# Kernel tuning notes

Measured on AMD Instinct MI355X. Metric: run time of the kernel, lower is better.

The kernel has to match this reference:

```python
import jax, jax.numpy as jnp
import numpy as np

B, N_REG, D_IN = 32, 116, 256
N_NODES = B * N_REG            # 3712
E_PER_G = N_REG * 10           # avg degree 10
E = B * E_PER_G                # 37120
HEADS = 8
HID = [256, 128, 64]
D_OUT = 256
LN_EPS = 1e-5


def _layer_norm(x, scale, bias):
    mu = x.mean(-1, keepdims=True)
    var = ((x - mu) ** 2).mean(-1, keepdims=True)
    return (x - mu) * jax.lax.rsqrt(var + LN_EPS) * scale + bias


def _gat_layer(x, W, b, a_src, a_dst, src, dst, concat):
    """PyG-style GATConv (shared lin, self-loops, leaky_relu 0.2) + ELU + LayerNorm."""
    N = x.shape[0]
    H, C = a_src.shape
    h = (x @ W).reshape(N, H, C)                      # (N, H, C)
    sl = jnp.arange(N, dtype=src.dtype)               # self-loops (PyG default)
    s = jnp.concatenate([src, sl])
    d = jnp.concatenate([dst, sl])
    al = (h * a_src).sum(-1)                          # (N, H)
    ar = (h * a_dst).sum(-1)                          # (N, H)
    e = jax.nn.leaky_relu(al[s] + ar[d], 0.2)         # (E', H)
    m = jax.ops.segment_max(e, d, num_segments=N)
    ex = jnp.exp(e - m[d])
    den = jax.ops.segment_sum(ex, d, num_segments=N)
    alpha = ex / den[d]                               # segment softmax over incoming edges
    out = jax.ops.segment_sum(h[s] * alpha[..., None], d, num_segments=N)  # (N, H, C)
    out = out.reshape(N, H * C) if concat else out.mean(1)
    return out + b


def setup_inputs() -> dict:
    key = jax.random.key(0)
    ks = list(jax.random.split(key, 32))
    node_features = jax.random.normal(ks[0], (N_NODES, D_IN), dtype=jnp.float32)
    # edges: random within each graph (disconnected batched graph)
    off = (jnp.arange(B, dtype=jnp.int32) * N_REG)[:, None]
    src = (jax.random.randint(ks[1], (B, E_PER_G), 0, N_REG, dtype=jnp.int32) + off).reshape(-1)
    dst = (jax.random.randint(ks[2], (B, E_PER_G), 0, N_REG, dtype=jnp.int32) + off).reshape(-1)
    batch = jnp.repeat(jnp.arange(B, dtype=jnp.int32), N_REG)

    def lin(k, fin, fout):
        s = 1.0 / np.sqrt(fin)
        return jax.random.uniform(k, (fin, fout), jnp.float32, -s, s)

    dims_in = [D_IN, HID[0] * HEADS, HID[1] * HEADS]
    p = {}
    ki = 3
    for i, (fin, c) in enumerate(zip(dims_in, HID)):
        concat = i < len(HID) - 1
        wdim = c * HEADS
        p[f"w{i}"] = lin(ks[ki], fin, wdim); ki += 1
        p[f"b{i}"] = jnp.zeros((wdim if concat else c,), jnp.float32)
        p[f"as{i}"] = jax.random.normal(ks[ki], (HEADS, c), jnp.float32) * 0.1; ki += 1
        p[f"ad{i}"] = jax.random.normal(ks[ki], (HEADS, c), jnp.float32) * 0.1; ki += 1
        ldim = wdim if concat else c
        p[f"ls{i}"] = jnp.ones((ldim,), jnp.float32)
        p[f"lb{i}"] = jnp.zeros((ldim,), jnp.float32)
    p["wp"] = lin(ks[ki], HID[-1], D_OUT); ki += 1
    p["bp"] = jnp.zeros((D_OUT,), jnp.float32)
    p["lsp"] = jnp.ones((D_OUT,), jnp.float32)
    p["lbp"] = jnp.zeros((D_OUT,), jnp.float32)
    p["wq"] = lin(ks[ki], D_OUT, 1); ki += 1
    p["bq"] = jnp.zeros((1,), jnp.float32)
    return dict(node_features=node_features, src=src, dst=dst, batch=batch, **p)


def reference(node_features, src, dst, batch,
              w0, b0, as0, ad0, ls0, lb0,
              w1, b1, as1, ad1, ls1, lb1,
              w2, b2, as2, ad2, ls2, lb2,
              wp, bp, lsp, lbp, wq, bq):
    x = node_features
    x = _layer_norm(jax.nn.elu(_gat_layer(x, w0, b0, as0, ad0, src, dst, True)), ls0, lb0)
    x = _layer_norm(jax.nn.elu(_gat_layer(x, w1, b1, as1, ad1, src, dst, True)), ls1, lb1)
    x = _layer_norm(jax.nn.elu(_gat_layer(x, w2, b2, as2, ad2, src, dst, False)), ls2, lb2)
    node_out = jax.nn.gelu(_layer_norm(x @ wp + bp, lsp, lbp), approximate=False)  # (N, 256)
    pool_w = jax.nn.softmax(node_out @ wq + bq, axis=0)                            # (N, 1) global softmax
    num = jax.ops.segment_sum(node_out * pool_w, batch, num_segments=B)            # (B, 256)
    den = jnp.maximum(jax.ops.segment_sum(pool_w, batch, num_segments=B), 1e-8)    # (B, 1)
    graph_features = num / den
    return graph_features, node_out
```

## Files before the change

### kernel.cpp

```cpp
#include <hip/hip_runtime.h>
#include <hip/hip_bf16.h>
#include <math.h>

typedef __hip_bfloat16 bf16;
typedef short short8 __attribute__((ext_vector_type(8)));
typedef float f32x4 __attribute__((ext_vector_type(4)));

__device__ __forceinline__ float b2f(const bf16 v) { return __bfloat162float(v); }
__device__ __forceinline__ bf16 f2b(const float v) { return __float2bfloat16(v); }

__device__ __forceinline__ float bits2f(short s) {
  unsigned u = ((unsigned)(unsigned short)s) << 16;
  float f;
  __builtin_memcpy(&f, &u, 4);
  return f;
}
__device__ __forceinline__ short f2bits(float f) {
  bf16 b = f2b(f);
  short s;
  __builtin_memcpy(&s, &b, 2);
  return s;
}

__device__ __forceinline__ float ldsel(const void* p, size_t i, int f32) {
  return f32 ? ((const float*)p)[i] : b2f(((const bf16*)p)[i]);
}
__device__ __forceinline__ void stsel(void* p, size_t i, float v, int f32) {
  if (f32) ((float*)p)[i] = v; else ((bf16*)p)[i] = f2b(v);
}

__device__ __forceinline__ void load8f(const void* p, int idx, int f32, float* o) {
  if (f32) {
    const float4* q = (const float4*)((const float*)p + idx);
    float4 a = q[0], b = q[1];
    o[0] = a.x; o[1] = a.y; o[2] = a.z; o[3] = a.w;
    o[4] = b.x; o[5] = b.y; o[6] = b.z; o[7] = b.w;
  } else {
    union { short8 v; short s[8]; } u;
    u.v = *(const short8*)((const bf16*)p + idx);
#pragma unroll
    for (int j = 0; j < 8; ++j) o[j] = bits2f(u.s[j]);
  }
}

#define NN 3712
#define NE 37120
#define NG 32
#define NREG 116
#define MAXDEG 48


__global__ __launch_bounds__(256) void k_detect(const void* nf, const void* w0, int* flags) {
  __shared__ int bad[2];
  if (threadIdx.x < 2) bad[threadIdx.x] = 0;
  __syncthreads();
  const bf16* a = (const bf16*)nf;
  const bf16* b = (const bf16*)w0;
  int l0 = 0, l1 = 0;
  for (int i = threadIdx.x; i < 4096; i += 256) {
    float x = b2f(a[i]); if (!(fabsf(x) < 1e4f)) l0++;
    float y = b2f(b[i]); if (!(fabsf(y) < 1e4f)) l1++;
  }
  if (l0) atomicAdd(&bad[0], l0);
  if (l1) atomicAdd(&bad[1], l1);
  __syncthreads();
  if (threadIdx.x == 0) { flags[0] = bad[0] > 0; flags[1] = bad[1] > 0; }
}

__global__ __launch_bounds__(256) void k_zero(int* __restrict__ p, int n) {
  int i = blockIdx.x * 256 + threadIdx.x;
  if (i < n) p[i] = 0;
}

__global__ __launch_bounds__(256) void k_scatter(const int* __restrict__ src, const int* __restrict__ dst,
                                                 int* __restrict__ cnt, int* __restrict__ bucket, int E) {
  int e = blockIdx.x * 256 + threadIdx.x;
  if (e < E) {
    int d = dst[e], s = src[e];
    if ((unsigned)d < NN && (unsigned)s < NN) {
      int p = atomicAdd(&cnt[d], 1);
      if (p < MAXDEG) bucket[d * MAXDEG + p] = s;
    }
  }
}

__global__ __launch_bounds__(256) void k_tox0(const void* __restrict__ in, bf16* __restrict__ out,
                                              const int* __restrict__ flags) {
  int f = flags[0];
  int bid = blockIdx.x;
  int n = (bid & 7) * 464 + (bid >> 3);
  int i = n * 256 + threadIdx.x;
  out[i] = f2b(ldsel(in, i, f));
}

__global__ __launch_bounds__(256) void k_transpose(const void* __restrict__ W, bf16* __restrict__ Wt,
                                                   int K, int N, const int* __restrict__ flags) {
  int f = flags[1];
  __shared__ float tile[32][33];
  int tx = threadIdx.x & 31, ty = threadIdx.x >> 5;
  int k0 = blockIdx.x * 32, n0 = blockIdx.y * 32;
#pragma unroll
  for (int i = 0; i < 4; ++i)
    tile[ty + i * 8][tx] = ldsel(W, (size_t)(k0 + ty + i * 8) * N + n0 + tx, f);
  __syncthreads();
#pragma unroll
  for (int i = 0; i < 4; ++i)
    Wt[(size_t)(n0 + ty + i * 8) * K + k0 + tx] = f2b(tile[tx][ty + i * 8]);
}

__global__ __launch_bounds__(256) void k_gemm_mfma(const bf16* __restrict__ A, const bf16* __restrict__ Bt,
                                                   bf16* __restrict__ C, int M, int N, int K) {
  __shared__ short As[64 * 72];
  __shared__ short Bs[64 * 72];
  int tid = threadIdx.x;
  int wave = tid >> 6, lane = tid & 63;
  int wr = wave >> 1, wc = wave & 1;
  int quad = lane >> 4, ml = lane & 15;

  int nbx = N >> 6;
  int total = gridDim.x;
  int id = blockIdx.x;
  int tile = ((total & 7) == 0) ? ((id & 7) * (total >> 3) + (id >> 3)) : id;
  int n0 = (tile % nbx) << 6;
  int m0 = (tile / nbx) << 6;

  f32x4 acc[2][2];
#pragma unroll
  for (int rt = 0; rt < 2; ++rt)
#pragma unroll
    for (int ct = 0; ct < 2; ++ct)
#pragma unroll
      for (int r = 0; r < 4; ++r) acc[rt][ct][r] = 0.f;

  for (int k0 = 0; k0 < K; k0 += 64) {
    __syncthreads();
#pragma unroll
    for (int i = 0; i < 2; ++i) {
      int c = tid + (i << 8);
      int row = c >> 3, kg = (c & 7) << 3;
      *(uint4*)&As[row * 72 + kg] = *(const uint4*)&A[(size_t)(m0 + row) * K + k0 + kg];
      *(uint4*)&Bs[row * 72 + kg] = *(const uint4*)&Bt[(size_t)(n0 + row) * K + k0 + kg];
    }
    __syncthreads();
    short8 af[2][2], bfr[2][2];
#pragma unroll
    for (int rt = 0; rt < 2; ++rt)
#pragma unroll
      for (int kk = 0; kk < 2; ++kk)
        af[rt][kk] = *(const short8*)&As[(wr * 32 + rt * 16 + ml) * 72 + kk * 32 + quad * 8];
#pragma unroll
    for (int ct = 0; ct < 2; ++ct)
#pragma unroll
      for (int kk = 0; kk < 2; ++kk)
        bfr[ct][kk] = *(const short8*)&Bs[(wc * 32 + ct * 16 + ml) * 72 + kk * 32 + quad * 8];
#pragma unroll
    for (int rt = 0; rt < 2; ++rt)
#pragma unroll
      for (int ct = 0; ct < 2; ++ct)
#pragma unroll
        for (int kk = 0; kk < 2; ++kk)
          acc[rt][ct] = __builtin_amdgcn_mfma_f32_16x16x32_bf16(af[rt][kk], bfr[ct][kk], acc[rt][ct], 0, 0, 0);
  }
#pragma unroll
  for (int rt = 0; rt < 2; ++rt)
#pragma unroll
    for (int ct = 0; ct < 2; ++ct)
#pragma unroll
      for (int r = 0; r < 4; ++r) {
        int grow = m0 + wr * 32 + rt * 16 + quad * 4 + r;
        int gcol = n0 + wc * 32 + ct * 16 + ml;
        C[(size_t)grow * N + gcol] = f2b(acc[rt][ct][r]);
      }
}

__global__ void k_attn(const bf16* __restrict__ H, const void* __restrict__ a_s,
                       const void* __restrict__ a_d, float* __restrict__ al,
                       float* __restrict__ ar, int C, const int* __restrict__ flags) {
  int wF = flags[1];
  int t = threadIdx.x;
  int D = 8 * C;
  int i0 = t * 8;
  int bid = blockIdx.x;
  int nb = (bid & 7) * 58 + (bid >> 3);
  float as8[8], ad8[8];
  load8f(a_s, i0, wF, as8);
  load8f(a_d, i0, wF, ad8);
  int G = C >> 3;
  int hd = i0 / C;
  for (int it = 0; it < 8; ++it) {
    int n = nb * 8 + it;
    union { short8 v; short s[8]; } u;
    u.v = *(const short8*)&H[(size_t)n * D + i0];
    float ps = 0.f, pd = 0.f;
#pragma unroll
    for (int j = 0; j < 8; ++j) {
      float h = bits2f(u.s[j]);
      ps = fmaf(h, as8[j], ps);
      pd = fmaf(h, ad8[j], pd);
    }
    for (int off = G >> 1; off; off >>= 1) {
      ps += __shfl_xor(ps, off);
      pd += __shfl_xor(pd, off);
    }
    if ((t & (G - 1)) == 0) {
      al[n * 8 + hd] = ps;
      ar[n * 8 + hd] = pd;
    }
  }
}

__global__ __launch_bounds__(256) void k_edgew(const float* __restrict__ al, const float* __restrict__ ar,
                                               const int* __restrict__ cnt, const int* __restrict__ bucket,
                                               float* __restrict__ mbuf, float* __restrict__ ibuf) {
  int t = threadIdx.x;
  int q = t >> 6, l = t & 63, hd = l >> 3, el = l & 7;
  int bid = blockIdx.x;
  int d = (bid & 7) * 464 + (bid >> 3) * 4 + q;
  int deg = cnt[d]; deg = deg > MAXDEG ? MAXDEG : deg;
  int total = deg + 1;
  float ard = ar[d * 8 + hd];
  float lgv[7];
  float m = -1e30f;
#pragma unroll
  for (int k = 0; k < 7; ++k) {
    int e = el + k * 8;
    float lg = -1e30f;
    if (e < total) {
      int s = e < deg ? bucket[d * MAXDEG + e] : d;
      lg = al[s * 8 + hd] + ard;
      lg = lg > 0.f ? lg : 0.2f * lg;
    }
    lgv[k] = lg;
    m = fmaxf(m, lg);
  }
#pragma unroll
  for (int off = 4; off; off >>= 1) m = fmaxf(m, __shfl_xor(m, off));
  float den = 0.f;
#pragma unroll
  for (int k = 0; k < 7; ++k) den += (lgv[k] > -1e29f) ? expf(lgv[k] - m) : 0.f;
#pragma unroll
  for (int off = 4; off; off >>= 1) den += __shfl_xor(den, off);
  if (el == 0) { mbuf[d * 8 + hd] = m; ibuf[d * 8 + hd] = 1.f / den; }
}

template<int C>
__global__ __launch_bounds__(256, 1) void k_aggm(const bf16* __restrict__ H,
    const float* __restrict__ al, const float* __restrict__ ar,
    const float* __restrict__ mbuf, const float* __restrict__ ibuf,
    const int* __restrict__ cnt, const int* __restrict__ bucket,
    bf16* __restrict__ Y) {
  constexpr int D = 8 * C;
  constexpr int KP = 136;
  __shared__ short P[128 * KP];
  __shared__ short Ht[C * KP];
  int t = threadIdx.x;
  int bid = blockIdx.x;
  int x = bid & 7, j = bid >> 3;
  int g = x * 4 + (j & 3);
  int h = j >> 2;
  int gbase = g * NREG;

  short8 z = {0, 0, 0, 0, 0, 0, 0, 0};
  for (int i = t; i < 128 * KP / 8; i += 256) *(short8*)&P[i * 8] = z;
  for (int i = t; i < C * 12; i += 256) {
    int c = i / 12, s = 116 + i % 12;
    Ht[c * KP + (s ^ (((c >> 3) & 15) << 3))] = 0;
  }
  __syncthreads();

  constexpr int CH = C / 8;
  for (int idx = t; idx < NREG * CH; idx += 256) {
    int s = idx / CH, c0 = (idx % CH) * 8;
    int msk = ((idx % CH) & 15) << 3;
    int sw = s ^ msk;
    union { short8 v; short x2[8]; } u;
    u.v = *(const short8*)&H[(size_t)(gbase + s) * D + h * C + c0];
#pragma unroll
    for (int jj = 0; jj < 8; ++jj) Ht[(c0 + jj) * KP + sw] = u.x2[jj];
  }
  if (t < NREG) {
    int gd = gbase + t;
    int deg = cnt[gd]; deg = deg > MAXDEG ? MAXDEG : deg;
    int total = deg + 1;
    float ard = ar[gd * 8 + h];
    float mm = mbuf[gd * 8 + h], inv = ibuf[gd * 8 + h];
    for (int base = 0; base < total; base += 8) {
      int sg[8]; float av[8];
#pragma unroll
      for (int jj = 0; jj < 8; ++jj) {
        int e = base + jj;
        sg[jj] = (e < deg) ? bucket[gd * MAXDEG + e] : gd;
      }
#pragma unroll
      for (int jj = 0; jj < 8; ++jj) av[jj] = al[sg[jj] * 8 + h];
#pragma unroll
      for (int jj = 0; jj < 8; ++jj) {
        if (base + jj < total) {
          float lg = av[jj] + ard;
          lg = lg > 0.f ? lg : 0.2f * lg;
          float alpha = expf(lg - mm) * inv;
          int off = t * KP + (sg[jj] - gbase);
          P[off] = f2bits(bits2f(P[off]) + alpha);
        }
      }
    }
  }
  __syncthreads();

  constexpr int CT = C / 32;
  int wave = t >> 6, lane = t & 63;
  int wr = wave >> 1, wc = wave & 1;
  int quad = lane >> 4, ml = lane & 15;
  f32x4 acc[4][CT];
#pragma unroll
  for (int a = 0; a < 4; ++a)
#pragma unroll
    for (int b = 0; b < CT; ++b)
#pragma unroll
      for (int r = 0; r < 4; ++r) acc[a][b][r] = 0.f;
#pragma unroll
  for (int ks = 0; ks < 4; ++ks) {
    short8 af[4], bf8[CT];
#pragma unroll
    for (int rt = 0; rt < 4; ++rt)
      af[rt] = *(const short8*)&P[(wr * 64 + rt * 16 + ml) * KP + ks * 32 + quad * 8];
#pragma unroll
    for (int ct = 0; ct < CT; ++ct) {
      int cdim = wc * (C / 2) + ct * 16 + ml;
      int msk = ((cdim >> 3) & 15) << 3;
      bf8[ct] = *(const short8*)&Ht[cdim * KP + ((ks * 32 + quad * 8) ^ msk)];
    }
#pragma unroll
    for (int rt = 0; rt < 4; ++rt)
#pragma unroll
      for (int ct = 0; ct < CT; ++ct)
        acc[rt][ct] = __builtin_amdgcn_mfma_f32_16x16x32_bf16(af[rt], bf8[ct], acc[rt][ct], 0, 0, 0);
  }
#pragma unroll
  for (int rt = 0; rt < 4; ++rt) {
    int m2 = wr * 64 + rt * 16 + quad * 4;
#pragma unroll
    for (int r = 0; r < 4; ++r) {
      if (m2 + r < NREG) {
#pragma unroll
        for (int ct = 0; ct < CT; ++ct) {
          int n = wc * (C / 2) + ct * 16 + ml;
          Y[(size_t)(gbase + m2 + r) * D + h * C + n] = f2b(acc[rt][ct][r]);
        }
      }
    }
  }
}

template<int D>
__global__ __launch_bounds__(256) void k_ln(bf16* __restrict__ X, const void* __restrict__ bias,
                                            const void* __restrict__ ls, const void* __restrict__ lb,
                                            const int* __restrict__ flags) {
  int wF = flags[1];
  constexpr int VPT = D / 256;
  int t = threadIdx.x;
  int bid = blockIdx.x;
  int nb = (bid & 7) * 58 + (bid >> 3);
  int node = nb * 8 + (t >> 5);
  int l32 = t & 31;
  float v[VPT * 8];
  float s1 = 0.f, s2 = 0.f;
#pragma unroll
  for (int j = 0; j < VPT; ++j) {
    int c0 = (l32 + j * 32) * 8;
    union { short8 u; short x[8]; } uu;
    uu.u = *(const short8*)&X[(size_t)node * D + c0];
    float bb[8];
    load8f(bias, c0, wF, bb);
#pragma unroll
    for (int k = 0; k < 8; ++k) {
      float vv = bits2f(uu.x[k]) + bb[k];
      vv = vv > 0.f ? vv : expf(vv) - 1.f;
      v[j * 8 + k] = vv; s1 += vv; s2 += vv * vv;
    }
  }
#pragma unroll
  for (int off = 16; off; off >>= 1) { s1 += __shfl_xor(s1, off); s2 += __shfl_xor(s2, off); }
  float mu = s1 / D;
  float rs = rsqrtf(s2 / D - mu * mu + 1e-5f);
#pragma unroll
  for (int j = 0; j < VPT; ++j) {
    int c0 = (l32 + j * 32) * 8;
    float g8[8], b8[8];
    load8f(ls, c0, wF, g8);
    load8f(lb, c0, wF, b8);
    union { short8 u; short x[8]; } uu;
#pragma unroll
    for (int k = 0; k < 8; ++k)
      uu.x[k] = f2bits((v[j * 8 + k] - mu) * rs * g8[k] + b8[k]);
    *(short8*)&X[(size_t)node * D + c0] = uu.u;
  }
}

__global__ void k_agg(const bf16* __restrict__ H, const float* __restrict__ al,
                      const float* __restrict__ ar, const float* __restrict__ mbuf,
                      const float* __restrict__ ibuf, const int* __restrict__ cnt,
                      const int* __restrict__ bucket, const void* __restrict__ bias,
                      const void* __restrict__ ls, const void* __restrict__ lb,
                      bf16* __restrict__ Xout, int C, int concat,
                      const int* __restrict__ flags) {
  int wF = flags[1];
  int bid = blockIdx.x;
  int d = (bid & 7) * 464 + (bid >> 3);
  int t = threadIdx.x;
  int D = 8 * C;
  __shared__ int sid[MAXDEG + 4];
  __shared__ float vals[512];

  int deg = cnt[d]; deg = deg > MAXDEG ? MAXDEG : deg;
  int total = deg + 1;
  int padded = (total + 3) & ~3;
  if (t < padded) sid[t] = t < deg ? bucket[d * MAXDEG + t] : d;
  __syncthreads();

  int i0 = t * 8;
  int hd = i0 / C;
  float m = mbuf[d * 8 + hd], inv = ibuf[d * 8 + hd], ard = ar[d * 8 + hd];

  float acc[8] = {0.f, 0.f, 0.f, 0.f, 0.f, 0.f, 0.f, 0.f};
  const bf16* __restrict__ Hp = H + i0;
  for (int eb = 0; eb < padded; eb += 4) {
    int s4[4]; float a4[4]; short8 u4[4];
#pragma unroll
    for (int j = 0; j < 4; ++j) s4[j] = sid[eb + j];
#pragma unroll
    for (int j = 0; j < 4; ++j) {
      a4[j] = al[s4[j] * 8 + hd];
      u4[j] = *(const short8*)&Hp[(size_t)s4[j] * D];
    }
#pragma unroll
    for (int j = 0; j < 4; ++j) {
      float lg = a4[j] + ard;
      lg = lg > 0.f ? lg : 0.2f * lg;
      float we = (eb + j) < total ? expf(lg - m) * inv : 0.f;
      union { short8 v; short s[8]; } uu; uu.v = u4[j];
#pragma unroll
      for (int k2 = 0; k2 < 8; ++k2) acc[k2] = fmaf(we, bits2f(uu.s[k2]), acc[k2]);
    }
  }

#pragma unroll
  for (int j = 0; j < 8; ++j) vals[i0 + j] = acc[j];
  __syncthreads();
  float v = 0.f;
#pragma unroll
  for (int h = 0; h < 8; ++h) v += vals[h * 64 + t];
  v = v * 0.125f + ldsel(bias, t, wF);
  v = v > 0.f ? v : expf(v) - 1.f;
  float s1 = v, s2 = v * v;
#pragma unroll
  for (int off = 32; off; off >>= 1) { s1 += __shfl_xor(s1, off); s2 += __shfl_xor(s2, off); }
  float mu = s1 * (1.f / 64.f);
  float var = s2 * (1.f / 64.f) - mu * mu;
  float rs = rsqrtf(var + 1e-5f);
  Xout[(size_t)d * 64 + t] = f2b((v - mu) * rs * ldsel(ls, t, wF) + ldsel(lb, t, wF));
}

__global__ __launch_bounds__(256) void k_proj(const bf16* __restrict__ X3, const void* __restrict__ wp,
                                              const void* __restrict__ bp, const void* __restrict__ lsp,
                                              const void* __restrict__ lbp, const void* __restrict__ wq,
                                              const void* __restrict__ bq,
                                              float* __restrict__ q, void* __restrict__ dout,
                                              const int* __restrict__ flags) {
  int wF = flags[1], xF = flags[0];
  int bid = blockIdx.x;
  int n = (bid & 7) * 464 + (bid >> 3);
  int t = threadIdx.x;
  int lane = t & 63, wave = t >> 6;
  __shared__ float xs[64];
  __shared__ float r1[4], r2[4];
  __shared__ float sMu, sRs;
  if (t < 64) xs[t] = b2f(X3[n * 64 + t]);
  __syncthreads();
  float y = ldsel(bp, t, wF);
#pragma unroll 8
  for (int k = 0; k < 64; ++k) y = fmaf(xs[k], ldsel(wp, k * 256 + t, wF), y);
  float s1 = y, s2 = y * y;
#pragma unroll
  for (int off = 32; off; off >>= 1) { s1 += __shfl_down(s1, off); s2 += __shfl_down(s2, off); }
  if (lane == 0) { r1[wave] = s1; r2[wave] = s2; }
  __syncthreads();
  if (t == 0) {
    float S1 = r1[0] + r1[1] + r1[2] + r1[3];
    float S2 = r2[0] + r2[1] + r2[2] + r2[3];
    float mu = S1 / 256.f;
    sMu = mu; sRs = rsqrtf(S2 / 256.f - mu * mu + 1e-5f);
  }
  __syncthreads();
  float v = (y - sMu) * sRs * ldsel(lsp, t, wF) + ldsel(lbp, t, wF);
  float g = 0.5f * v * (1.f + erff(v * 0.70710678118654752f));
  stsel(dout, (size_t)NG * 256 + (size_t)n * 256 + t, g, xF);
  float qv = g * ldsel(wq, t, wF);
#pragma unroll
  for (int off = 32; off; off >>= 1) qv += __shfl_down(qv, off);
  if (lane == 0) r1[wave] = qv;
  __syncthreads();
  if (t == 0) q[n] = r1[0] + r1[1] + r1[2] + r1[3] + ldsel(bq, 0, wF);
}

__global__ __launch_bounds__(256) void k_pool(void* __restrict__ dout, const float* __restrict__ q,
                                              const int* __restrict__ flags) {
  int xF = flags[0];
  int bid = blockIdx.x;
  int b = (bid & 7) * 4 + (bid >> 3);
  int t = threadIdx.x;
  __shared__ float es[NREG];
  __shared__ float sDen;
  if (t < NREG) es[t] = q[b * NREG + t];
  __syncthreads();
  if (t == 0) {
    float m = -1e30f;
    for (int i = 0; i < NREG; ++i) m = fmaxf(m, es[i]);
    float den = 0.f;
    for (int i = 0; i < NREG; ++i) { float e = expf(es[i] - m); es[i] = e; den += e; }
    sDen = den;
  }
  __syncthreads();
  float acc = 0.f;
  for (int i = 0; i < NREG; ++i)
    acc = fmaf(es[i], ldsel(dout, (size_t)NG * 256 + (size_t)(b * NREG + i) * 256 + t, xF), acc);
  stsel(dout, (size_t)b * 256 + t, acc / sDen, xF);
}

extern "C" void kernel_launch(void* const* d_in, const int* in_sizes, int n_in,
                              void* d_out, int out_size, void* d_ws, size_t ws_size,
                              hipStream_t stream) {
  const void* nf  = d_in[0];
  const int* src  = (const int*)d_in[1];
  const int* dst  = (const int*)d_in[2];
  const void *w0 = d_in[4],  *b0 = d_in[5],  *as0 = d_in[6], *ad0 = d_in[7],  *ls0 = d_in[8],  *lb0 = d_in[9];
  const void *w1 = d_in[10], *b1 = d_in[11], *as1 = d_in[12], *ad1 = d_in[13], *ls1 = d_in[14], *lb1 = d_in[15];
  const void *w2 = d_in[16], *b2 = d_in[17], *as2 = d_in[18], *ad2 = d_in[19], *ls2 = d_in[20], *lb2 = d_in[21];
  const void *wp = d_in[22], *bp = d_in[23], *lsp = d_in[24], *lbp = d_in[25], *wq = d_in[26], *bq = d_in[27];

  int* flags  = (int*)d_ws;
  float* al   = (float*)(flags + 4);
  float* ar   = al + NN * 8;
  int* cnt    = (int*)(ar + NN * 8);
  int* bucket = cnt + NN;
  float* q    = (float*)(bucket + NN * MAXDEG);
  bf16* X     = (bf16*)(q + NN);
  bf16* Hb    = X + (size_t)NN * 2048;

  float* mbuf = (float*)d_out;
  float* ibuf = mbuf + NN * 8;

  bf16* X0  = X;
  bf16* wt0 = X + (1 << 20);
  bf16* wt1 = Hb + (size_t)NN * 1024;
  bf16* wt2 = Hb + (size_t)NN * 512;

  k_detect<<<1, 256, 0, stream>>>(nf, w0, flags);
  k_zero<<<(NN + 255) / 256, 256, 0, stream>>>(cnt, NN);
  k_scatter<<<(NE + 255) / 256, 256, 0, stream>>>(src, dst, cnt, bucket, NE);
  k_tox0<<<NN, 256, 0, stream>>>(nf, X0, flags);

  k_transpose<<<dim3(256 / 32, 2048 / 32), 256, 0, stream>>>(w0, wt0, 256, 2048, flags);
  k_gemm_mfma<<<(2048 / 64) * (NN / 64), 256, 0, stream>>>(X0, wt0, Hb, NN, 2048, 256);
  k_attn<<<NN / 8, 256, 0, stream>>>(Hb, as0, ad0, al, ar, 256, flags);
  k_edgew<<<NN / 4, 256, 0, stream>>>(al, ar, cnt, bucket, mbuf, ibuf);
  k_aggm<256><<<256, 256, 0, stream>>>(Hb, al, ar, mbuf, ibuf, cnt, bucket, X);
  k_ln<2048><<<NN / 8, 256, 0, stream>>>(X, b0, ls0, lb0, flags);

  k_transpose<<<dim3(2048 / 32, 1024 / 32), 256, 0, stream>>>(w1, wt1, 2048, 1024, flags);
  k_gemm_mfma<<<(1024 / 64) * (NN / 64), 256, 0, stream>>>(X, wt1, Hb, NN, 1024, 2048);
  k_attn<<<NN / 8, 128, 0, stream>>>(Hb, as1, ad1, al, ar, 128, flags);
  k_edgew<<<NN / 4, 256, 0, stream>>>(al, ar, cnt, bucket, mbuf, ibuf);
  k_aggm<128><<<256, 256, 0, stream>>>(Hb, al, ar, mbuf, ibuf, cnt, bucket, X);
  k_ln<1024><<<NN / 8, 256, 0, stream>>>(X, b1, ls1, lb1, flags);

  k_transpose<<<dim3(1024 / 32, 512 / 32), 256, 0, stream>>>(w2, wt2, 1024, 512, flags);
  k_gemm_mfma<<<(512 / 64) * (NN / 64), 256, 0, stream>>>(X, wt2, Hb, NN, 512, 1024);
  k_attn<<<NN / 8, 64, 0, stream>>>(Hb, as2, ad2, al, ar, 64, flags);
  k_edgew<<<NN / 4, 256, 0, stream>>>(al, ar, cnt, bucket, mbuf, ibuf);
  k_agg<<<NN, 64, 0, stream>>>(Hb, al, ar, mbuf, ibuf, cnt, bucket, b2, ls2, lb2, X, 64, 0, flags);

  k_proj<<<NN, 256, 0, stream>>>(X, wp, bp, lsp, lbp, wq, bq, q, d_out, flags);
  k_pool<<<NG, 256, 0, stream>>>(d_out, q, flags);
}
```

Baseline: 329.7 us.

## Fuse attention-logit reduction into GEMM epilogue and merge prep kernels

Computes the per-head attention logits (al/ar) inside the GEMM epilogue from the fp32 accumulators, using shuffles and atomicAdd into zeroed buffers. This removes the separate k_attn pass that re-read the projected features. The setup kernels (detect, zero, scatter, convert, transpose) are merged into two launches, and the next layer's weight transpose plus the al/ar zeroing are folded into the LayerNorm launch. The aim is fewer launches and less memory traffic, at the cost of float atomics, non-deterministic summation order, and logits taken from unrounded fp32 accumulators rather than bf16 values.

```diff
diff --git a/kernel.cpp b/kernel.cpp
--- a/kernel.cpp
+++ b/kernel.cpp
@@ -50,55 +50,33 @@
 #define MAXDEG 48
 
 
-__global__ __launch_bounds__(256) void k_detect(const void* nf, const void* w0, int* flags) {
-  __shared__ int bad[2];
-  if (threadIdx.x < 2) bad[threadIdx.x] = 0;
-  __syncthreads();
-  const bf16* a = (const bf16*)nf;
-  const bf16* b = (const bf16*)w0;
-  int l0 = 0, l1 = 0;
-  for (int i = threadIdx.x; i < 4096; i += 256) {
-    float x = b2f(a[i]); if (!(fabsf(x) < 1e4f)) l0++;
-    float y = b2f(b[i]); if (!(fabsf(y) < 1e4f)) l1++;
-  }
-  if (l0) atomicAdd(&bad[0], l0);
-  if (l1) atomicAdd(&bad[1], l1);
-  __syncthreads();
-  if (threadIdx.x == 0) { flags[0] = bad[0] > 0; flags[1] = bad[1] > 0; }
-}
-
-__global__ __launch_bounds__(256) void k_zero(int* __restrict__ p, int n) {
-  int i = blockIdx.x * 256 + threadIdx.x;
-  if (i < n) p[i] = 0;
-}
-
-__global__ __launch_bounds__(256) void k_scatter(const int* __restrict__ src, const int* __restrict__ dst,
-                                                 int* __restrict__ cnt, int* __restrict__ bucket, int E) {
-  int e = blockIdx.x * 256 + threadIdx.x;
-  if (e < E) {
-    int d = dst[e], s = src[e];
-    if ((unsigned)d < NN && (unsigned)s < NN) {
-      int p = atomicAdd(&cnt[d], 1);
-      if (p < MAXDEG) bucket[d * MAXDEG + p] = s;
-    }
-  }
-}
-
-__global__ __launch_bounds__(256) void k_tox0(const void* __restrict__ in, bf16* __restrict__ out,
-                                              const int* __restrict__ flags) {
-  int f = flags[0];
-  int bid = blockIdx.x;
-  int n = (bid & 7) * 464 + (bid >> 3);
-  int i = n * 256 + threadIdx.x;
-  out[i] = f2b(ldsel(in, i, f));
-}
-
-__global__ __launch_bounds__(256) void k_transpose(const void* __restrict__ W, bf16* __restrict__ Wt,
-                                                   int K, int N, const int* __restrict__ flags) {
-  int f = flags[1];
-  __shared__ float tile[32][33];
+__global__ __launch_bounds__(256) void k_prep1(const void* nf, const void* w0,
+                                               int* flags, int* cnt) {
+  if (blockIdx.x == 0) {
+    __shared__ int bad[2];
+    if (threadIdx.x < 2) bad[threadIdx.x] = 0;
+    __syncthreads();
+    const bf16* a = (const bf16*)nf;
+    const bf16* b = (const bf16*)w0;
+    int l0 = 0, l1 = 0;
+    for (int i = threadIdx.x; i < 4096; i += 256) {
+      float x = b2f(a[i]); if (!(fabsf(x) < 1e4f)) l0++;
+      float y = b2f(b[i]); if (!(fabsf(y) < 1e4f)) l1++;
+    }
+    if (l0) atomicAdd(&bad[0], l0);
+    if (l1) atomicAdd(&bad[1], l1);
+    __syncthreads();
+    if (threadIdx.x == 0) { flags[0] = bad[0] > 0; flags[1] = bad[1] > 0; }
+  } else {
+    int i = (blockIdx.x - 1) * 256 + threadIdx.x;
+    if (i < NN) cnt[i] = 0;
+  }
+}
+
+__device__ __forceinline__ void dev_transpose(const void* W, bf16* Wt, int K, int N,
+                                              int bx, int by, int f, float tile[32][33]) {
   int tx = threadIdx.x & 31, ty = threadIdx.x >> 5;
-  int k0 = blockIdx.x * 32, n0 = blockIdx.y * 32;
+  int k0 = bx * 32, n0 = by * 32;
 #pragma unroll
   for (int i = 0; i < 4; ++i)
     tile[ty + i * 8][tx] = ldsel(W, (size_t)(k0 + ty + i * 8) * N + n0 + tx, f);
@@ -108,8 +86,40 @@
     Wt[(size_t)(n0 + ty + i * 8) * K + k0 + tx] = f2b(tile[tx][ty + i * 8]);
 }
 
+__global__ __launch_bounds__(256) void k_prep2(const int* __restrict__ src, const int* __restrict__ dst,
+    int* __restrict__ cnt, int* __restrict__ bucket, const void* __restrict__ nf, bf16* __restrict__ X0,
+    const void* __restrict__ w0, bf16* __restrict__ wt0, float* __restrict__ al, float* __restrict__ ar,
+    const int* __restrict__ flags) {
+  __shared__ float tile[32][33];
+  int id = blockIdx.x, t = threadIdx.x;
+  if (id < 145) {
+    int e = id * 256 + t;
+    if (e < NE) {
+      int d = dst[e], s = src[e];
+      if ((unsigned)d < NN && (unsigned)s < NN) {
+        int p = atomicAdd(&cnt[d], 1);
+        if (p < MAXDEG) bucket[d * MAXDEG + p] = s;
+      }
+    }
+  } else if ((id -= 145) < NN) {
+    int f = flags[0];
+    int n = (id & 7) * 464 + (id >> 3);
+    int i = n * 256 + t;
+    X0[i] = f2b(ldsel(nf, i, f));
+  } else if ((id -= NN) < 512) {
+    dev_transpose(w0, wt0, 256, 2048, id & 7, id >> 3, flags[1], tile);
+  } else {
+    id -= 512;
+    int i = id * 256 + t;
+    if (i < NN * 8) { al[i] = 0.f; ar[i] = 0.f; }
+  }
+}
+
 __global__ __launch_bounds__(256) void k_gemm_mfma(const bf16* __restrict__ A, const bf16* __restrict__ Bt,
-                                                   bf16* __restrict__ C, int M, int N, int K) {
+                                                   bf16* __restrict__ C, int M, int N, int K,
+                                                   const void* __restrict__ a_s, const void* __restrict__ a_d,
+                                                   float* __restrict__ al, float* __restrict__ ar,
+                                                   int Chead, const int* __restrict__ flags) {
   __shared__ short As[64 * 72];
   __shared__ short Bs[64 * 72];
   int tid = threadIdx.x;
@@ -171,41 +181,46 @@
         int gcol = n0 + wc * 32 + ct * 16 + ml;
         C[(size_t)grow * N + gcol] = f2b(acc[rt][ct][r]);
       }
-}
-
-__global__ void k_attn(const bf16* __restrict__ H, const void* __restrict__ a_s,
-                       const void* __restrict__ a_d, float* __restrict__ al,
-                       float* __restrict__ ar, int C, const int* __restrict__ flags) {
+
   int wF = flags[1];
-  int t = threadIdx.x;
-  int D = 8 * C;
-  int i0 = t * 8;
-  int bid = blockIdx.x;
-  int nb = (bid & 7) * 58 + (bid >> 3);
-  float as8[8], ad8[8];
-  load8f(a_s, i0, wF, as8);
-  load8f(a_d, i0, wF, ad8);
-  int G = C >> 3;
-  int hd = i0 / C;
-  for (int it = 0; it < 8; ++it) {
-    int n = nb * 8 + it;
-    union { short8 v; short s[8]; } u;
-    u.v = *(const short8*)&H[(size_t)n * D + i0];
-    float ps = 0.f, pd = 0.f;
-#pragma unroll
-    for (int j = 0; j < 8; ++j) {
-      float h = bits2f(u.s[j]);
-      ps = fmaf(h, as8[j], ps);
-      pd = fmaf(h, ad8[j], pd);
-    }
-    for (int off = G >> 1; off; off >>= 1) {
-      ps += __shfl_xor(ps, off);
-      pd += __shfl_xor(pd, off);
-    }
-    if ((t & (G - 1)) == 0) {
-      al[n * 8 + hd] = ps;
-      ar[n * 8 + hd] = pd;
-    }
+  int hd = n0 / Chead;
+  float asv[2], adv[2];
+#pragma unroll
+  for (int ct = 0; ct < 2; ++ct) {
+    int gcol = n0 + wc * 32 + ct * 16 + ml;
+    asv[ct] = ldsel(a_s, gcol, wF);
+    adv[ct] = ldsel(a_d, gcol, wF);
+  }
+  float pal[8], par[8];
+#pragma unroll
+  for (int k = 0; k < 8; ++k) { pal[k] = 0.f; par[k] = 0.f; }
+#pragma unroll
+  for (int rt = 0; rt < 2; ++rt)
+#pragma unroll
+    for (int ct = 0; ct < 2; ++ct)
+#pragma unroll
+      for (int r = 0; r < 4; ++r) {
+        int k = rt * 4 + r;
+        pal[k] = fmaf(acc[rt][ct][r], asv[ct], pal[k]);
+        par[k] = fmaf(acc[rt][ct][r], adv[ct], par[k]);
+      }
+#pragma unroll
+  for (int off = 1; off < 16; off <<= 1) {
+#pragma unroll
+    for (int k = 0; k < 8; ++k) {
+      pal[k] += __shfl_xor(pal[k], off);
+      par[k] += __shfl_xor(par[k], off);
+    }
+  }
+  if (ml == 0) {
+#pragma unroll
+    for (int rt = 0; rt < 2; ++rt)
+#pragma unroll
+      for (int r = 0; r < 4; ++r) {
+        int grow = m0 + wr * 32 + rt * 16 + quad * 4 + r;
+        atomicAdd(&al[grow * 8 + hd], pal[rt * 4 + r]);
+        atomicAdd(&ar[grow * 8 + hd], par[rt * 4 + r]);
+      }
   }
 }
 
@@ -352,14 +367,24 @@
   }
 }
 
-template<int D>
+template<int D, int TK, int TN>
 __global__ __launch_bounds__(256) void k_ln(bf16* __restrict__ X, const void* __restrict__ bias,
                                             const void* __restrict__ ls, const void* __restrict__ lb,
+                                            float* __restrict__ al, float* __restrict__ ar,
+                                            const void* __restrict__ W, bf16* __restrict__ Wt,
                                             const int* __restrict__ flags) {
+  __shared__ float tile[32][33];
+  int bid = blockIdx.x;
+  if (bid >= 464) {
+    int id = bid - 464;
+    dev_transpose(W, Wt, TK, TN, id % (TK / 32), id / (TK / 32), flags[1], tile);
+    return;
+  }
+  int gid = bid * 256 + threadIdx.x;
+  if (gid < NN * 8) { al[gid] = 0.f; ar[gid] = 0.f; }
   int wF = flags[1];
   constexpr int VPT = D / 256;
   int t = threadIdx.x;
-  int bid = blockIdx.x;
   int nb = (bid & 7) * 58 + (bid >> 3);
   int node = nb * 8 + (t >> 5);
   int l32 = t & 31;
@@ -555,28 +580,24 @@
   bf16* wt1 = Hb + (size_t)NN * 1024;
   bf16* wt2 = Hb + (size_t)NN * 512;
 
-  k_detect<<<1, 256, 0, stream>>>(nf, w0, flags);
-  k_zero<<<(NN + 255) / 256, 256, 0, stream>>>(cnt, NN);
-  k_scatter<<<(NE + 255) / 256, 256, 0, stream>>>(src, dst, cnt, bucket, NE);
-  k_tox0<<<NN, 256, 0, stream>>>(nf, X0, flags);
-
-  k_transpose<<<dim3(256 / 32, 2048 / 32), 256, 0, stream>>>(w0, wt0, 256, 2048, flags);
-  k_gemm_mfma<<<(2048 / 64) * (NN / 64), 256, 0, stream>>>(X0, wt0, Hb, NN, 2048, 256);
-  k_attn<<<NN / 8, 256, 0, stream>>>(Hb, as0, ad0, al, ar, 256, flags);
+  k_prep1<<<1 + (NN + 255) / 256, 256, 0, stream>>>(nf, w0, flags, cnt);
+  k_prep2<<<145 + NN + 512 + 116, 256, 0, stream>>>(
+      src, dst, cnt, bucket, nf, X0, w0, wt0, al, ar, flags);
+
+  k_gemm_mfma<<<(2048 / 64) * (NN / 64), 256, 0, stream>>>(X0, wt0, Hb, NN, 2048, 256,
+                                                           as0, ad0, al, ar, 256, flags);
   k_edgew<<<NN / 4, 256, 0, stream>>>(al, ar, cnt, bucket, mbuf, ibuf);
   k_aggm<256><<<256, 256, 0, stream>>>(Hb, al, ar, mbuf, ibuf, cnt, bucket, X);
-  k_ln<2048><<<NN / 8, 256, 0, stream>>>(X, b0, ls0, lb0, flags);
-
-  k_transpose<<<dim3(2048 / 32, 1024 / 32), 256, 0, stream>>>(w1, wt1, 2048, 1024, flags);
-  k_gemm_mfma<<<(1024 / 64) * (NN / 64), 256, 0, stream>>>(X, wt1, Hb, NN, 1024, 2048);
-  k_attn<<<NN / 8, 128, 0, stream>>>(Hb, as1, ad1, al, ar, 128, flags);
+  k_ln<2048, 2048, 1024><<<464 + 2048, 256, 0, stream>>>(X, b0, ls0, lb0, al, ar, w1, wt1, flags);
+
+  k_gemm_mfma<<<(1024 / 64) * (NN / 64), 256, 0, stream>>>(X, wt1, Hb, NN, 1024, 2048,
+                                                           as1, ad1, al, ar, 128, flags);
   k_edgew<<<NN / 4, 256, 0, stream>>>(al, ar, cnt, bucket, mbuf, ibuf);
   k_aggm<128><<<256, 256, 0, stream>>>(Hb, al, ar, mbuf, ibuf, cnt, bucket, X);
-  k_ln<1024><<<NN / 8, 256, 0, stream>>>(X, b1, ls1, lb1, flags);
-
-  k_transpose<<<dim3(1024 / 32, 512 / 32), 256, 0, stream>>>(w2, wt2, 1024, 512, flags);
-  k_gemm_mfma<<<(512 / 64) * (NN / 64), 256, 0, stream>>>(X, wt2, Hb, NN, 512, 1024);
-  k_attn<<<NN / 8, 64, 0, stream>>>(Hb, as2, ad2, al, ar, 64, flags);
+  k_ln<1024, 1024, 512><<<464 + 512, 256, 0, stream>>>(X, b1, ls1, lb1, al, ar, w2, wt2, flags);
+
+  k_gemm_mfma<<<(512 / 64) * (NN / 64), 256, 0, stream>>>(X, wt2, Hb, NN, 512, 1024,
+                                                          as2, ad2, al, ar, 64, flags);
   k_edgew<<<NN / 4, 256, 0, stream>>>(al, ar, cnt, bucket, mbuf, ibuf);
   k_agg<<<NN, 64, 0, stream>>>(Hb, al, ar, mbuf, ibuf, cnt, bucket, b2, ls2, lb2, X, 64, 0, flags);
 
```

Result: slower. 341.1 us (+3.5%).

## Merge prep and transpose kernels into fewer launches and deepen GEMM K-tile

Applied to the files above, without the earlier changes.

Merges detect and zero into one launch, and scatter, input conversion and the w0 transpose into a second launch split by block index. The w1 and w2 transposes become extra blocks on the preceding layer-norm launches. This cuts the launch count and lets independent small work share a launch. Separately, the MFMA GEMM now stages a 128-wide K slice per iteration instead of 64, halving barrier and loop overhead at the cost of more shared memory per block and possibly lower occupancy.

```diff
diff --git a/kernel.cpp b/kernel.cpp
--- a/kernel.cpp
+++ b/kernel.cpp
@@ -50,55 +50,33 @@
 #define MAXDEG 48
 
 
-__global__ __launch_bounds__(256) void k_detect(const void* nf, const void* w0, int* flags) {
-  __shared__ int bad[2];
-  if (threadIdx.x < 2) bad[threadIdx.x] = 0;
-  __syncthreads();
-  const bf16* a = (const bf16*)nf;
-  const bf16* b = (const bf16*)w0;
-  int l0 = 0, l1 = 0;
-  for (int i = threadIdx.x; i < 4096; i += 256) {
-    float x = b2f(a[i]); if (!(fabsf(x) < 1e4f)) l0++;
-    float y = b2f(b[i]); if (!(fabsf(y) < 1e4f)) l1++;
-  }
-  if (l0) atomicAdd(&bad[0], l0);
-  if (l1) atomicAdd(&bad[1], l1);
-  __syncthreads();
-  if (threadIdx.x == 0) { flags[0] = bad[0] > 0; flags[1] = bad[1] > 0; }
-}
-
-__global__ __launch_bounds__(256) void k_zero(int* __restrict__ p, int n) {
-  int i = blockIdx.x * 256 + threadIdx.x;
-  if (i < n) p[i] = 0;
-}
-
-__global__ __launch_bounds__(256) void k_scatter(const int* __restrict__ src, const int* __restrict__ dst,
-                                                 int* __restrict__ cnt, int* __restrict__ bucket, int E) {
-  int e = blockIdx.x * 256 + threadIdx.x;
-  if (e < E) {
-    int d = dst[e], s = src[e];
-    if ((unsigned)d < NN && (unsigned)s < NN) {
-      int p = atomicAdd(&cnt[d], 1);
-      if (p < MAXDEG) bucket[d * MAXDEG + p] = s;
-    }
-  }
-}
-
-__global__ __launch_bounds__(256) void k_tox0(const void* __restrict__ in, bf16* __restrict__ out,
-                                              const int* __restrict__ flags) {
-  int f = flags[0];
-  int bid = blockIdx.x;
-  int n = (bid & 7) * 464 + (bid >> 3);
-  int i = n * 256 + threadIdx.x;
-  out[i] = f2b(ldsel(in, i, f));
-}
-
-__global__ __launch_bounds__(256) void k_transpose(const void* __restrict__ W, bf16* __restrict__ Wt,
-                                                   int K, int N, const int* __restrict__ flags) {
-  int f = flags[1];
-  __shared__ float tile[32][33];
+__global__ __launch_bounds__(256) void k_prep1(const void* nf, const void* w0,
+                                               int* flags, int* cnt) {
+  if (blockIdx.x == 0) {
+    __shared__ int bad[2];
+    if (threadIdx.x < 2) bad[threadIdx.x] = 0;
+    __syncthreads();
+    const bf16* a = (const bf16*)nf;
+    const bf16* b = (const bf16*)w0;
+    int l0 = 0, l1 = 0;
+    for (int i = threadIdx.x; i < 4096; i += 256) {
+      float x = b2f(a[i]); if (!(fabsf(x) < 1e4f)) l0++;
+      float y = b2f(b[i]); if (!(fabsf(y) < 1e4f)) l1++;
+    }
+    if (l0) atomicAdd(&bad[0], l0);
+    if (l1) atomicAdd(&bad[1], l1);
+    __syncthreads();
+    if (threadIdx.x == 0) { flags[0] = bad[0] > 0; flags[1] = bad[1] > 0; }
+  } else {
+    int i = (blockIdx.x - 1) * 256 + threadIdx.x;
+    if (i < NN) cnt[i] = 0;
+  }
+}
+
+__device__ __forceinline__ void dev_transpose(const void* W, bf16* Wt, int K, int N,
+                                              int bx, int by, int f, float tile[32][33]) {
   int tx = threadIdx.x & 31, ty = threadIdx.x >> 5;
-  int k0 = blockIdx.x * 32, n0 = blockIdx.y * 32;
+  int k0 = bx * 32, n0 = by * 32;
 #pragma unroll
   for (int i = 0; i < 4; ++i)
     tile[ty + i * 8][tx] = ldsel(W, (size_t)(k0 + ty + i * 8) * N + n0 + tx, f);
@@ -108,10 +86,35 @@
     Wt[(size_t)(n0 + ty + i * 8) * K + k0 + tx] = f2b(tile[tx][ty + i * 8]);
 }
 
+__global__ __launch_bounds__(256) void k_prep2(const int* __restrict__ src, const int* __restrict__ dst,
+    int* __restrict__ cnt, int* __restrict__ bucket, const void* __restrict__ nf, bf16* __restrict__ X0,
+    const void* __restrict__ w0, bf16* __restrict__ wt0, const int* __restrict__ flags) {
+  __shared__ float tile[32][33];
+  int id = blockIdx.x, t = threadIdx.x;
+  if (id < 145) {
+    int e = id * 256 + t;
+    if (e < NE) {
+      int d = dst[e], s = src[e];
+      if ((unsigned)d < NN && (unsigned)s < NN) {
+        int p = atomicAdd(&cnt[d], 1);
+        if (p < MAXDEG) bucket[d * MAXDEG + p] = s;
+      }
+    }
+  } else if ((id -= 145) < NN) {
+    int f = flags[0];
+    int n = (id & 7) * 464 + (id >> 3);
+    int i = n * 256 + t;
+    X0[i] = f2b(ldsel(nf, i, f));
+  } else {
+    id -= NN;
+    dev_transpose(w0, wt0, 256, 2048, id & 7, id >> 3, flags[1], tile);
+  }
+}
+
 __global__ __launch_bounds__(256) void k_gemm_mfma(const bf16* __restrict__ A, const bf16* __restrict__ Bt,
                                                    bf16* __restrict__ C, int M, int N, int K) {
-  __shared__ short As[64 * 72];
-  __shared__ short Bs[64 * 72];
+  __shared__ short As[64 * 136];
+  __shared__ short Bs[64 * 136];
   int tid = threadIdx.x;
   int wave = tid >> 6, lane = tid & 63;
   int wr = wave >> 1, wc = wave & 1;
@@ -132,33 +135,33 @@
 #pragma unroll
       for (int r = 0; r < 4; ++r) acc[rt][ct][r] = 0.f;
 
-  for (int k0 = 0; k0 < K; k0 += 64) {
+  for (int k0 = 0; k0 < K; k0 += 128) {
     __syncthreads();
 #pragma unroll
-    for (int i = 0; i < 2; ++i) {
+    for (int i = 0; i < 4; ++i) {
       int c = tid + (i << 8);
-      int row = c >> 3, kg = (c & 7) << 3;
-      *(uint4*)&As[row * 72 + kg] = *(const uint4*)&A[(size_t)(m0 + row) * K + k0 + kg];
-      *(uint4*)&Bs[row * 72 + kg] = *(const uint4*)&Bt[(size_t)(n0 + row) * K + k0 + kg];
+      int row = c >> 4, kg = (c & 15) << 3;
+      *(uint4*)&As[row * 136 + kg] = *(const uint4*)&A[(size_t)(m0 + row) * K + k0 + kg];
+      *(uint4*)&Bs[row * 136 + kg] = *(const uint4*)&Bt[(size_t)(n0 + row) * K + k0 + kg];
     }
     __syncthreads();
-    short8 af[2][2], bfr[2][2];
+    short8 af[2][4], bfr[2][4];
 #pragma unroll
     for (int rt = 0; rt < 2; ++rt)
 #pragma unroll
-      for (int kk = 0; kk < 2; ++kk)
-        af[rt][kk] = *(const short8*)&As[(wr * 32 + rt * 16 + ml) * 72 + kk * 32 + quad * 8];
+      for (int kk = 0; kk < 4; ++kk)
+        af[rt][kk] = *(const short8*)&As[(wr * 32 + rt * 16 + ml) * 136 + kk * 32 + quad * 8];
 #pragma unroll
     for (int ct = 0; ct < 2; ++ct)
 #pragma unroll
-      for (int kk = 0; kk < 2; ++kk)
-        bfr[ct][kk] = *(const short8*)&Bs[(wc * 32 + ct * 16 + ml) * 72 + kk * 32 + quad * 8];
+      for (int kk = 0; kk < 4; ++kk)
+        bfr[ct][kk] = *(const short8*)&Bs[(wc * 32 + ct * 16 + ml) * 136 + kk * 32 + quad * 8];
 #pragma unroll
     for (int rt = 0; rt < 2; ++rt)
 #pragma unroll
       for (int ct = 0; ct < 2; ++ct)
 #pragma unroll
-        for (int kk = 0; kk < 2; ++kk)
+        for (int kk = 0; kk < 4; ++kk)
           acc[rt][ct] = __builtin_amdgcn_mfma_f32_16x16x32_bf16(af[rt][kk], bfr[ct][kk], acc[rt][ct], 0, 0, 0);
   }
 #pragma unroll
@@ -352,14 +355,21 @@
   }
 }
 
-template<int D>
+template<int D, int TK, int TN>
 __global__ __launch_bounds__(256) void k_ln(bf16* __restrict__ X, const void* __restrict__ bias,
                                             const void* __restrict__ ls, const void* __restrict__ lb,
+                                            const void* __restrict__ W, bf16* __restrict__ Wt,
                                             const int* __restrict__ flags) {
+  __shared__ float tile[32][33];
+  int bid = blockIdx.x;
+  if (bid >= 464) {
+    int id = bid - 464;
+    dev_transpose(W, Wt, TK, TN, id % (TK / 32), id / (TK / 32), flags[1], tile);
+    return;
+  }
   int wF = flags[1];
   constexpr int VPT = D / 256;
   int t = threadIdx.x;
-  int bid = blockIdx.x;
   int nb = (bid & 7) * 58 + (bid >> 3);
   int node = nb * 8 + (t >> 5);
   int l32 = t & 31;
@@ -555,26 +565,21 @@
   bf16* wt1 = Hb + (size_t)NN * 1024;
   bf16* wt2 = Hb + (size_t)NN * 512;
 
-  k_detect<<<1, 256, 0, stream>>>(nf, w0, flags);
-  k_zero<<<(NN + 255) / 256, 256, 0, stream>>>(cnt, NN);
-  k_scatter<<<(NE + 255) / 256, 256, 0, stream>>>(src, dst, cnt, bucket, NE);
-  k_tox0<<<NN, 256, 0, stream>>>(nf, X0, flags);
-
-  k_transpose<<<dim3(256 / 32, 2048 / 32), 256, 0, stream>>>(w0, wt0, 256, 2048, flags);
+  k_prep1<<<1 + (NN + 255) / 256, 256, 0, stream>>>(nf, w0, flags, cnt);
+  k_prep2<<<145 + NN + 512, 256, 0, stream>>>(src, dst, cnt, bucket, nf, X0, w0, wt0, flags);
+
   k_gemm_mfma<<<(2048 / 64) * (NN / 64), 256, 0, stream>>>(X0, wt0, Hb, NN, 2048, 256);
   k_attn<<<NN / 8, 256, 0, stream>>>(Hb, as0, ad0, al, ar, 256, flags);
   k_edgew<<<NN / 4, 256, 0, stream>>>(al, ar, cnt, bucket, mbuf, ibuf);
   k_aggm<256><<<256, 256, 0, stream>>>(Hb, al, ar, mbuf, ibuf, cnt, bucket, X);
-  k_ln<2048><<<NN / 8, 256, 0, stream>>>(X, b0, ls0, lb0, flags);
-
-  k_transpose<<<dim3(2048 / 32, 1024 / 32), 256, 0, stream>>>(w1, wt1, 2048, 1024, flags);
+  k_ln<2048, 2048, 1024><<<464 + 2048, 256, 0, stream>>>(X, b0, ls0, lb0, w1, wt1, flags);
+
   k_gemm_mfma<<<(1024 / 64) * (NN / 64), 256, 0, stream>>>(X, wt1, Hb, NN, 1024, 2048);
   k_attn<<<NN / 8, 128, 0, stream>>>(Hb, as1, ad1, al, ar, 128, flags);
   k_edgew<<<NN / 4, 256, 0, stream>>>(al, ar, cnt, bucket, mbuf, ibuf);
   k_aggm<128><<<256, 256, 0, stream>>>(Hb, al, ar, mbuf, ibuf, cnt, bucket, X);
-  k_ln<1024><<<NN / 8, 256, 0, stream>>>(X, b1, ls1, lb1, flags);
-
-  k_transpose<<<dim3(1024 / 32, 512 / 32), 256, 0, stream>>>(w2, wt2, 1024, 512, flags);
+  k_ln<1024, 1024, 512><<<464 + 512, 256, 0, stream>>>(X, b1, ls1, lb1, w2, wt2, flags);
+
   k_gemm_mfma<<<(512 / 64) * (NN / 64), 256, 0, stream>>>(X, wt2, Hb, NN, 512, 1024);
   k_attn<<<NN / 8, 64, 0, stream>>>(Hb, as2, ad2, al, ar, 64, flags);
   k_edgew<<<NN / 4, 256, 0, stream>>>(al, ar, cnt, bucket, mbuf, ibuf);
```

After: 311.9 us. 1.06x faster.
